# Kernel tuning notes

Hardware: AMD Instinct MI355X
Metric: run time of the kernel (lower is better)

## Reference

```python
import jax, jax.numpy as jnp
import numpy as np

N, E, F, C, K, H = 100000, 1600000, 64, 32, 8, 36


def setup_inputs() -> dict:
    key = jax.random.key(0)
    ks = jax.random.split(key, 24)
    s = 0.1
    inp = {
        "x": jax.random.normal(ks[0], (N, F), jnp.float32),
        "edge_index": jax.random.randint(ks[1], (2, E), 0, N, dtype=jnp.int32),
        # ChebConv conv1_1: K x [F, H] weights + bias
        "W1_1": jax.random.normal(ks[2], (K, F, H), jnp.float32) * s,
        "b1_1": jnp.zeros((H,), jnp.float32),
        "g1_1": jnp.ones((H,), jnp.float32),
        "be1_1": jnp.zeros((H,), jnp.float32),
        # ChebConv conv1_2: K x [H, H]
        "W1_2": jax.random.normal(ks[3], (K, H, H), jnp.float32) * s,
        "b1_2": jnp.zeros((H,), jnp.float32),
        "g1_2": jnp.ones((H,), jnp.float32),
        "be1_2": jnp.zeros((H,), jnp.float32),
        # GINConv MLP: Linear(F,H) -> ReLU -> Linear(H,H)
        "gin_w1": jax.random.normal(ks[4], (F, H), jnp.float32) * s,
        "gin_b1": jnp.zeros((H,), jnp.float32),
        "gin_w2": jax.random.normal(ks[5], (H, H), jnp.float32) * s,
        "gin_b2": jnp.zeros((H,), jnp.float32),
        "g2": jnp.ones((H,), jnp.float32),
        "be2": jnp.zeros((H,), jnp.float32),
        # conv4: ChebConv K=1 on concat(3H) -> C  (pure linear, no propagation)
        "W4": jax.random.normal(ks[6], (1, 3 * H, C), jnp.float32) * s,
        "b4": jnp.zeros((C,), jnp.float32),
    }
    return inp


def _spmm(w, src, dst, x, n):
    # out[i] = sum_{e: dst_e=i} w_e * x[src_e]
    return jax.ops.segment_sum(w[:, None] * x[src], dst, num_segments=n)


def _cheb(x, src, dst, w, Wk, b):
    # PyG ChebConv with sym norm, lambda_max=2: L_hat = -D^-1/2 A D^-1/2 (loop weight 0)
    n = x.shape[0]
    Kk = Wk.shape[0]
    Tx0 = x
    out = Tx0 @ Wk[0]
    if Kk > 1:
        Tx1 = _spmm(w, src, dst, Tx0, n)
        out = out + Tx1 @ Wk[1]
        for k in range(2, Kk):
            Tx2 = 2.0 * _spmm(w, src, dst, Tx1, n) - Tx0
            out = out + Tx2 @ Wk[k]
            Tx0, Tx1 = Tx1, Tx2
    return out + b


def _bn(x, g, b, eps=1e-5):
    m = jnp.mean(x, axis=0)
    v = jnp.mean(jnp.square(x - m), axis=0)  # biased var, training-mode BN
    return g * (x - m) * jax.lax.rsqrt(v + eps) + b


def reference(x, edge_index, W1_1, b1_1, g1_1, be1_1, W1_2, b1_2, g1_2, be1_2,
              gin_w1, gin_b1, gin_w2, gin_b2, g2, be2, W4, b4):
    src, dst = edge_index[0], edge_index[1]
    n = x.shape[0]
    deg = jax.ops.segment_sum(jnp.ones((src.shape[0],), x.dtype), src, num_segments=n)
    dis = jnp.where(deg > 0, jax.lax.rsqrt(jnp.maximum(deg, 1.0)), 0.0)
    w = -dis[src] * dis[dst]  # scaled Laplacian edge weights

    x1_1 = jax.nn.relu(_bn(_cheb(x, src, dst, w, W1_1, b1_1), g1_1, be1_1))
    x1_2 = jax.nn.relu(_bn(_cheb(x1_1, src, dst, w, W1_2, b1_2), g1_2, be1_2))

    # GINConv (eps=0): nn(x + sum_{j in N(i)} x_j)
    agg = jax.ops.segment_sum(x[src], dst, num_segments=n)
    h = x + agg
    gin = jax.nn.relu(h @ gin_w1 + gin_b1) @ gin_w2 + gin_b2
    x2 = _bn(jax.nn.relu(gin), g2, be2)

    x4 = jnp.concatenate((x1_1, x1_2, x2), axis=1)
    return x4 @ W4[0] + b4
```

## Files before the change

### kernel.cpp

```cpp
#include <hip/hip_runtime.h>

constexpr int N_NODES = 100000;
constexpr int N_EDGES = 1600000;
constexpr int NBK  = 391;
constexpr int NBLK = 640;
constexpr int CHUNK = 2500;
constexpr int LCNT = NBK * NBLK;
constexpr int SCAN_BLKS = (LCNT + 255) / 256;


__device__ __forceinline__ unsigned bf16pack(float a, float b) {
    unsigned ua = __float_as_uint(a), ub = __float_as_uint(b);
    ua += 0x7fffu + ((ua >> 16) & 1u);
    ub += 0x7fffu + ((ub >> 16) & 1u);
    return (ua >> 16) | (ub & 0xffff0000u);
}
__device__ __forceinline__ float bflo(unsigned p) { return __uint_as_float(p << 16); }
__device__ __forceinline__ float bfhi(unsigned p) { return __uint_as_float(p & 0xffff0000u); }


__global__ __launch_bounds__(256) void part_count_kernel(
    const int* __restrict__ ei, int* __restrict__ cntD, int* __restrict__ cntS) {
    __shared__ int hd[NBK], hs[NBK];
    int tid = threadIdx.x;
    for (int i = tid; i < NBK; i += 256) { hd[i] = 0; hs[i] = 0; }
    __syncthreads();
    int e0 = blockIdx.x * CHUNK;
    for (int e = e0 + tid; e < e0 + CHUNK; e += 256) {
        int s = ei[e], d = ei[N_EDGES + e];
        atomicAdd(&hs[s >> 8], 1);
        atomicAdd(&hd[d >> 8], 1);
    }
    __syncthreads();
    for (int i = tid; i < NBK; i += 256) {
        cntD[i * NBLK + blockIdx.x] = hd[i];
        cntS[i * NBLK + blockIdx.x] = hs[i];
    }
}

__global__ __launch_bounds__(256) void scanA_kernel(const int* __restrict__ in,
                                                    int* __restrict__ out,
                                                    int* __restrict__ bsum, int L) {
    __shared__ int sm[256];
    int i = blockIdx.x * 256 + threadIdx.x;
    int v = (i < L) ? in[i] : 0;
    sm[threadIdx.x] = v;
    __syncthreads();
    for (int off = 1; off < 256; off <<= 1) {
        int t = (threadIdx.x >= off) ? sm[threadIdx.x - off] : 0;
        __syncthreads();
        sm[threadIdx.x] += t;
        __syncthreads();
    }
    if (i < L) out[i] = sm[threadIdx.x] - v;
    if (threadIdx.x == 255) bsum[blockIdx.x] = sm[255];
}

__global__ __launch_bounds__(1024) void scanB_kernel(int* __restrict__ bsum, int nb) {
    __shared__ int sm[1024];
    int t = threadIdx.x;
    int v = (t < nb) ? bsum[t] : 0;
    sm[t] = v;
    __syncthreads();
    for (int off = 1; off < 1024; off <<= 1) {
        int u = (t >= off) ? sm[t - off] : 0;
        __syncthreads();
        sm[t] += u;
        __syncthreads();
    }
    if (t < nb) bsum[t] = sm[t] - v;
}

__global__ __launch_bounds__(256) void scanC_kernel(int* __restrict__ out,
                                                    const int* __restrict__ bsum, int L) {
    int i = blockIdx.x * 256 + threadIdx.x;
    if (i < L) out[i] += bsum[blockIdx.x];
}

__global__ __launch_bounds__(256) void part_scatter_kernel(
    const int* __restrict__ ei, const int* __restrict__ scanD,
    const int* __restrict__ scanS, int2* __restrict__ edgepart,
    int* __restrict__ srcpart) {
    __shared__ int curD[NBK], curS[NBK];
    int tid = threadIdx.x;
    for (int i = tid; i < NBK; i += 256) {
        curD[i] = scanD[i * NBLK + blockIdx.x];
        curS[i] = scanS[i * NBLK + blockIdx.x];
    }
    __syncthreads();
    int e0 = blockIdx.x * CHUNK;
    for (int e = e0 + tid; e < e0 + CHUNK; e += 256) {
        int s = ei[e], d = ei[N_EDGES + e];
        int pd = atomicAdd(&curD[d >> 8], 1);
        edgepart[pd] = make_int2(s, d);
        int ps = atomicAdd(&curS[s >> 8], 1);
        srcpart[ps] = s;
    }
}

__global__ __launch_bounds__(256) void deg_kernel(const int* __restrict__ srcpart,
                                                  const int* __restrict__ scanS,
                                                  float* __restrict__ dis) {
    __shared__ int cnt[256];
    int b = blockIdx.x, tid = threadIdx.x;
    cnt[tid] = 0;
    __syncthreads();
    int beg = scanS[b * NBLK];
    int end = (b + 1 < NBK) ? scanS[(b + 1) * NBLK] : N_EDGES;
    for (int j = beg + tid; j < end; j += 256)
        atomicAdd(&cnt[srcpart[j] & 255], 1);
    __syncthreads();
    int node = b * 256 + tid;
    if (node < N_NODES) dis[node] = cnt[tid] > 0 ? rsqrtf((float)cnt[tid]) : 0.f;
}

__global__ __launch_bounds__(256) void csr_kernel(const int2* __restrict__ edgepart,
                                                  const int* __restrict__ scanD,
                                                  const float* __restrict__ dis,
                                                  int* __restrict__ rp,
                                                  int2* __restrict__ csrw) {
    __shared__ int cnt[256];
    __shared__ int lofs[256];
    __shared__ float disl[256];
    int b = blockIdx.x, tid = threadIdx.x;
    int beg = scanD[b * NBLK];
    int end = (b + 1 < NBK) ? scanD[(b + 1) * NBLK] : N_EDGES;
    int node = b * 256 + tid;
    cnt[tid] = 0;
    disl[tid] = (node < N_NODES) ? dis[node] : 0.f;
    __syncthreads();
    for (int j = beg + tid; j < end; j += 256)
        atomicAdd(&cnt[edgepart[j].y & 255], 1);
    __syncthreads();
    int v = cnt[tid];
    lofs[tid] = v;
    __syncthreads();
    for (int off = 1; off < 256; off <<= 1) {
        int t = (tid >= off) ? lofs[tid - off] : 0;
        __syncthreads();
        lofs[tid] += t;
        __syncthreads();
    }
    int myexc = lofs[tid] - v;
    if (node < N_NODES) rp[node] = beg + myexc;
    if (b == NBK - 1 && tid == 0) rp[N_NODES] = N_EDGES;
    __syncthreads();
    lofs[tid] = myexc;
    cnt[tid] = 0;
    __syncthreads();
    for (int j = beg + tid; j < end; j += 256) {
        int2 e = edgepart[j];
        int dl = e.y & 255;
        int pos = beg + lofs[dl] + atomicAdd(&cnt[dl], 1);
        csrw[pos] = make_int2(e.x, __float_as_int(-dis[e.x] * disl[dl]));
    }
}


template <int FI, int SCALE, bool HAS_B2, bool BN_A, bool FUSE_STATS, bool OUT_BF16>
__global__ __launch_bounds__(256) void cheb_step_kernel(
    const int* __restrict__ rp, const int2* __restrict__ csrw,
    const uint2* __restrict__ INb, const uint2* __restrict__ B2b,
    const float* __restrict__ A, const float* __restrict__ W,
    const float* __restrict__ ss, void* __restrict__ OUT,
    float* __restrict__ partials) {
    __shared__ float Wl[FI * 36];
    __shared__ float Atile[28][FI + 1];
    __shared__ float ls[72];
    int tid = threadIdx.x;
    for (int i = tid; i < FI * 36; i += 252) Wl[i] = W[i];
    int r0 = blockIdx.x * 28;
    for (int i = tid; i < 28 * FI; i += 252) {
        int r = i / FI, f = i % FI;
        int row = r0 + r;
        float v = (row < N_NODES) ? A[row * FI + f] : 0.f;
        if (BN_A) v = fmaxf(fmaf(ss[f], v, ss[36 + f]), 0.f);
        Atile[r][f] = v;
    }
    if (FUSE_STATS && tid < 72) ls[tid] = 0.f;
    __syncthreads();
    int r = tid / 9, c = tid % 9;
    int row = r0 + r;
    bool valid = row < N_NODES;
    float ax = 0, ay = 0, az = 0, aw = 0;
    float bx = 0, by = 0, bz = 0, bw = 0;
    float cx = 0, cy = 0, cz = 0, cw = 0;
    float dx = 0, dy = 0, dz = 0, dw = 0;
    if (SCALE != 0 && valid) {
        int beg = rp[row], end = rp[row + 1];
        int j = beg;
        for (; j + 7 < end; j += 8) {
            int2 e0 = csrw[j],     e1 = csrw[j + 1], e2 = csrw[j + 2], e3 = csrw[j + 3];
            int2 e4 = csrw[j + 4], e5 = csrw[j + 5], e6 = csrw[j + 6], e7 = csrw[j + 7];
            uint2 u0 = INb[e0.x * 9 + c];
            uint2 u1 = INb[e1.x * 9 + c];
            uint2 u2 = INb[e2.x * 9 + c];
            uint2 u3 = INb[e3.x * 9 + c];
            uint2 u4 = INb[e4.x * 9 + c];
            uint2 u5 = INb[e5.x * 9 + c];
            uint2 u6 = INb[e6.x * 9 + c];
            uint2 u7 = INb[e7.x * 9 + c];
            float w0 = __int_as_float(e0.y), w1 = __int_as_float(e1.y);
            float w2 = __int_as_float(e2.y), w3 = __int_as_float(e3.y);
            float w4 = __int_as_float(e4.y), w5 = __int_as_float(e5.y);
            float w6 = __int_as_float(e6.y), w7 = __int_as_float(e7.y);
            ax = fmaf(w0, bflo(u0.x), ax); ay = fmaf(w0, bfhi(u0.x), ay);
            az = fmaf(w0, bflo(u0.y), az); aw = fmaf(w0, bfhi(u0.y), aw);
            bx = fmaf(w1, bflo(u1.x), bx); by = fmaf(w1, bfhi(u1.x), by);
            bz = fmaf(w1, bflo(u1.y), bz); bw = fmaf(w1, bfhi(u1.y), bw);
            cx = fmaf(w2, bflo(u2.x), cx); cy = fmaf(w2, bfhi(u2.x), cy);
            cz = fmaf(w2, bflo(u2.y), cz); cw = fmaf(w2, bfhi(u2.y), cw);
            dx = fmaf(w3, bflo(u3.x), dx); dy = fmaf(w3, bfhi(u3.x), dy);
            dz = fmaf(w3, bflo(u3.y), dz); dw = fmaf(w3, bfhi(u3.y), dw);
            ax = fmaf(w4, bflo(u4.x), ax); ay = fmaf(w4, bfhi(u4.x), ay);
            az = fmaf(w4, bflo(u4.y), az); aw = fmaf(w4, bfhi(u4.y), aw);
            bx = fmaf(w5, bflo(u5.x), bx); by = fmaf(w5, bfhi(u5.x), by);
            bz = fmaf(w5, bflo(u5.y), bz); bw = fmaf(w5, bfhi(u5.y), bw);
            cx = fmaf(w6, bflo(u6.x), cx); cy = fmaf(w6, bfhi(u6.x), cy);
            cz = fmaf(w6, bflo(u6.y), cz); cw = fmaf(w6, bfhi(u6.y), cw);
            dx = fmaf(w7, bflo(u7.x), dx); dy = fmaf(w7, bfhi(u7.x), dy);
            dz = fmaf(w7, bflo(u7.y), dz); dw = fmaf(w7, bfhi(u7.y), dw);
        }
        for (; j + 3 < end; j += 4) {
            int2 e0 = csrw[j], e1 = csrw[j + 1], e2 = csrw[j + 2], e3 = csrw[j + 3];
            uint2 u0 = INb[e0.x * 9 + c];
            uint2 u1 = INb[e1.x * 9 + c];
            uint2 u2 = INb[e2.x * 9 + c];
            uint2 u3 = INb[e3.x * 9 + c];
            float w0 = __int_as_float(e0.y), w1 = __int_as_float(e1.y);
            float w2 = __int_as_float(e2.y), w3 = __int_as_float(e3.y);
            ax = fmaf(w0, bflo(u0.x), ax); ay = fmaf(w0, bfhi(u0.x), ay);
            az = fmaf(w0, bflo(u0.y), az); aw = fmaf(w0, bfhi(u0.y), aw);
            bx = fmaf(w1, bflo(u1.x), bx); by = fmaf(w1, bfhi(u1.x), by);
            bz = fmaf(w1, bflo(u1.y), bz); bw = fmaf(w1, bfhi(u1.y), bw);
            cx = fmaf(w2, bflo(u2.x), cx); cy = fmaf(w2, bfhi(u2.x), cy);
            cz = fmaf(w2, bflo(u2.y), cz); cw = fmaf(w2, bfhi(u2.y), cw);
            dx = fmaf(w3, bflo(u3.x), dx); dy = fmaf(w3, bfhi(u3.x), dy);
            dz = fmaf(w3, bflo(u3.y), dz); dw = fmaf(w3, bfhi(u3.y), dw);
        }
        for (; j < end; ++j) {
            int2 e = csrw[j];
            uint2 u = INb[e.x * 9 + c];
            float w = __int_as_float(e.y);
            ax = fmaf(w, bflo(u.x), ax); ay = fmaf(w, bfhi(u.x), ay);
            az = fmaf(w, bflo(u.y), az); aw = fmaf(w, bfhi(u.y), aw);
        }
        ax += bx + cx + dx; ay += by + cy + dy;
        az += bz + cz + dz; aw += bw + cw + dw;
    }
    float px = 0, py = 0, pz = 0, pw = 0;
    const float4* Wl4 = (const float4*)Wl;
#pragma unroll 4
    for (int f = 0; f < FI; ++f) {
        float a = Atile[r][f];
        float4 wv = Wl4[f * 9 + c];
        px = fmaf(a, wv.x, px); py = fmaf(a, wv.y, py);
        pz = fmaf(a, wv.z, pz); pw = fmaf(a, wv.w, pw);
    }
    const float S = (float)SCALE;
    float4 o;
    o.x = fmaf(S, ax, px); o.y = fmaf(S, ay, py);
    o.z = fmaf(S, az, pz); o.w = fmaf(S, aw, pw);
    if (valid) {
        if (HAS_B2) {
            uint2 u = B2b[row * 9 + c];
            o.x -= bflo(u.x); o.y -= bfhi(u.x);
            o.z -= bflo(u.y); o.w -= bfhi(u.y);
        }
        if (OUT_BF16) {
            ((uint2*)OUT)[row * 9 + c] =
                make_uint2(bf16pack(o.x, o.y), bf16pack(o.z, o.w));
        } else {
            ((float4*)OUT)[row * 9 + c] = o;
        }
        if (FUSE_STATS) {
            atomicAdd(&ls[c * 4 + 0], o.x); atomicAdd(&ls[36 + c * 4 + 0], o.x * o.x);
            atomicAdd(&ls[c * 4 + 1], o.y); atomicAdd(&ls[36 + c * 4 + 1], o.y * o.y);
            atomicAdd(&ls[c * 4 + 2], o.z); atomicAdd(&ls[36 + c * 4 + 2], o.z * o.z);
            atomicAdd(&ls[c * 4 + 3], o.w); atomicAdd(&ls[36 + c * 4 + 3], o.w * o.w);
        }
    }
    if (FUSE_STATS) {
        __syncthreads();
        if (tid < 72) partials[blockIdx.x * 72 + tid] = ls[tid];
    }
}


__global__ __launch_bounds__(256) void gin_gather_kernel(
    const int* __restrict__ rp, const int2* __restrict__ csrw,
    const uint2* __restrict__ Yb, const float* __restrict__ b1,
    const float* __restrict__ w2, const float* __restrict__ b2,
    float* __restrict__ OUT, float* __restrict__ partials) {
    __shared__ float W2l[36 * 36];
    __shared__ float B1l[36], B2l[36];
    __shared__ float M1t[28][37];
    __shared__ float ls[72];
    int tid = threadIdx.x;
    for (int i = tid; i < 36 * 36; i += 252) W2l[i] = w2[i];
    if (tid < 36) { B1l[tid] = b1[tid]; B2l[tid] = b2[tid]; }
    if (tid < 72) ls[tid] = 0.f;
    __syncthreads();
    int r = tid / 9, c = tid % 9;
    int row = blockIdx.x * 28 + r;
    bool valid = row < N_NODES;
    float ax = 0, ay = 0, az = 0, aw = 0;
    float bx = 0, by = 0, bz = 0, bw = 0;
    float cx = 0, cy = 0, cz = 0, cw = 0;
    float dx = 0, dy = 0, dz = 0, dw = 0;
    if (valid) {
        uint2 us = Yb[row * 9 + c];
        ax = bflo(us.x); ay = bfhi(us.x); az = bflo(us.y); aw = bfhi(us.y);
        int beg = rp[row], end = rp[row + 1];
        int j = beg;
        for (; j + 7 < end; j += 8) {
            int s0 = csrw[j].x,     s1 = csrw[j + 1].x, s2 = csrw[j + 2].x, s3 = csrw[j + 3].x;
            int s4 = csrw[j + 4].x, s5 = csrw[j + 5].x, s6 = csrw[j + 6].x, s7 = csrw[j + 7].x;
            uint2 u0 = Yb[s0 * 9 + c];
            uint2 u1 = Yb[s1 * 9 + c];
            uint2 u2 = Yb[s2 * 9 + c];
            uint2 u3 = Yb[s3 * 9 + c];
            uint2 u4 = Yb[s4 * 9 + c];
            uint2 u5 = Yb[s5 * 9 + c];
            uint2 u6 = Yb[s6 * 9 + c];
            uint2 u7 = Yb[s7 * 9 + c];
            ax += bflo(u0.x) + bflo(u4.x); ay += bfhi(u0.x) + bfhi(u4.x);
            az += bflo(u0.y) + bflo(u4.y); aw += bfhi(u0.y) + bfhi(u4.y);
            bx += bflo(u1.x) + bflo(u5.x); by += bfhi(u1.x) + bfhi(u5.x);
            bz += bflo(u1.y) + bflo(u5.y); bw += bfhi(u1.y) + bfhi(u5.y);
            cx += bflo(u2.x) + bflo(u6.x); cy += bfhi(u2.x) + bfhi(u6.x);
            cz += bflo(u2.y) + bflo(u6.y); cw += bfhi(u2.y) + bfhi(u6.y);
            dx += bflo(u3.x) + bflo(u7.x); dy += bfhi(u3.x) + bfhi(u7.x);
            dz += bflo(u3.y) + bflo(u7.y); dw += bfhi(u3.y) + bfhi(u7.y);
        }
        for (; j + 3 < end; j += 4) {
            int s0 = csrw[j].x, s1 = csrw[j + 1].x, s2 = csrw[j + 2].x, s3 = csrw[j + 3].x;
            uint2 u0 = Yb[s0 * 9 + c];
            uint2 u1 = Yb[s1 * 9 + c];
            uint2 u2 = Yb[s2 * 9 + c];
            uint2 u3 = Yb[s3 * 9 + c];
            ax += bflo(u0.x); ay += bfhi(u0.x); az += bflo(u0.y); aw += bfhi(u0.y);
            bx += bflo(u1.x); by += bfhi(u1.x); bz += bflo(u1.y); bw += bfhi(u1.y);
            cx += bflo(u2.x); cy += bfhi(u2.x); cz += bflo(u2.y); cw += bfhi(u2.y);
            dx += bflo(u3.x); dy += bfhi(u3.x); dz += bflo(u3.y); dw += bfhi(u3.y);
        }
        for (; j < end; ++j) {
            uint2 u = Yb[csrw[j].x * 9 + c];
            ax += bflo(u.x); ay += bfhi(u.x);
            az += bflo(u.y); aw += bfhi(u.y);
        }
        ax += bx + cx + dx; ay += by + cy + dy;
        az += bz + cz + dz; aw += bw + cw + dw;
    }
    float m0 = fmaxf(ax + B1l[c * 4 + 0], 0.f);
    float m1 = fmaxf(ay + B1l[c * 4 + 1], 0.f);
    float m2 = fmaxf(az + B1l[c * 4 + 2], 0.f);
    float m3 = fmaxf(aw + B1l[c * 4 + 3], 0.f);
    M1t[r][c * 4 + 0] = m0; M1t[r][c * 4 + 1] = m1;
    M1t[r][c * 4 + 2] = m2; M1t[r][c * 4 + 3] = m3;
    __syncthreads();
    float o0 = B2l[c * 4 + 0], o1 = B2l[c * 4 + 1];
    float o2 = B2l[c * 4 + 2], o3 = B2l[c * 4 + 3];
    const float4* W2l4 = (const float4*)W2l;
#pragma unroll 4
    for (int f = 0; f < 36; ++f) {
        float a = M1t[r][f];
        float4 wv = W2l4[f * 9 + c];
        o0 = fmaf(a, wv.x, o0); o1 = fmaf(a, wv.y, o1);
        o2 = fmaf(a, wv.z, o2); o3 = fmaf(a, wv.w, o3);
    }
    o0 = fmaxf(o0, 0.f); o1 = fmaxf(o1, 0.f);
    o2 = fmaxf(o2, 0.f); o3 = fmaxf(o3, 0.f);
    if (valid) {
        float4 o = {o0, o1, o2, o3};
        ((float4*)OUT)[row * 9 + c] = o;
        atomicAdd(&ls[c * 4 + 0], o0); atomicAdd(&ls[36 + c * 4 + 0], o0 * o0);
        atomicAdd(&ls[c * 4 + 1], o1); atomicAdd(&ls[36 + c * 4 + 1], o1 * o1);
        atomicAdd(&ls[c * 4 + 2], o2); atomicAdd(&ls[36 + c * 4 + 2], o2 * o2);
        atomicAdd(&ls[c * 4 + 3], o3); atomicAdd(&ls[36 + c * 4 + 3], o3 * o3);
    }
    __syncthreads();
    if (tid < 72) partials[blockIdx.x * 72 + tid] = ls[tid];
}


__global__ __launch_bounds__(256) void finalize_kernel(
    const float* __restrict__ partials, int nb, const float* __restrict__ g,
    const float* __restrict__ be, float* __restrict__ ss) {
    __shared__ float rs[256], rq[256];
    int c = blockIdx.x;
    int t = threadIdx.x;
    float s = 0.f, q = 0.f;
    for (int i = t; i < nb; i += 256) {
        s += partials[i * 72 + c];
        q += partials[i * 72 + c + 36];
    }
    rs[t] = s; rq[t] = q;
    __syncthreads();
    for (int off = 128; off > 0; off >>= 1) {
        if (t < off) { rs[t] += rs[t + off]; rq[t] += rq[t + off]; }
        __syncthreads();
    }
    if (t == 0) {
        float m = rs[0] / (float)N_NODES;
        float v = rq[0] / (float)N_NODES - m * m;
        float sc = g[c] * rsqrtf(v + 1e-5f);
        ss[c] = sc;
        ss[36 + c] = be[c] - m * sc;
    }
}


__global__ __launch_bounds__(256) void fused3_kernel(
    const float* __restrict__ X1, const float* __restrict__ ssA,
    const float* __restrict__ X2, const float* __restrict__ ssB,
    const float* __restrict__ X3, const float* __restrict__ ssC,
    const float* __restrict__ W, const float* __restrict__ b,
    float* __restrict__ out) {
    __shared__ float Wl[108 * 32];
    __shared__ float Al[64][109];
    int tid = threadIdx.x;
    for (int i = tid; i < 108 * 32; i += 256) Wl[i] = W[i];
    int r0 = blockIdx.x * 64;
    for (int i = tid; i < 64 * 108; i += 256) {
        int r = i / 108, f = i % 108;
        int row = r0 + r;
        float v = 0.f;
        if (row < N_NODES) {
            if (f < 36) {
                v = fmaxf(fmaf(ssA[f], X1[row * 36 + f], ssA[36 + f]), 0.f);
            } else if (f < 72) {
                int ff = f - 36;
                v = fmaxf(fmaf(ssB[ff], X2[row * 36 + ff], ssB[36 + ff]), 0.f);
            } else {
                int ff = f - 72;
                v = fmaf(ssC[ff], X3[row * 36 + ff], ssC[36 + ff]);
            }
        }
        Al[r][f] = v;
    }
    __syncthreads();
    int r = tid >> 2, q = tid & 3;
    int row = r0 + r;
    if (row >= N_NODES) return;
    float acc[8];
#pragma unroll
    for (int j = 0; j < 8; ++j) acc[j] = b[q * 8 + j];
    for (int f = 0; f < 108; ++f) {
        float a = Al[r][f];
#pragma unroll
        for (int j = 0; j < 8; ++j)
            acc[j] = fmaf(a, Wl[f * 32 + q * 8 + j], acc[j]);
    }
#pragma unroll
    for (int j = 0; j < 8; ++j) out[row * 32 + q * 8 + j] = acc[j];
}


extern "C" void kernel_launch(void* const* d_in, const int* in_sizes, int n_in,
                              void* d_out, int out_size, void* d_ws, size_t ws_size,
                              hipStream_t stream) {
    const float* x      = (const float*)d_in[0];
    const int*   ei     = (const int*)d_in[1];
    const float* W1_1   = (const float*)d_in[2];
    const float* g1_1   = (const float*)d_in[4];
    const float* be1_1  = (const float*)d_in[5];
    const float* W1_2   = (const float*)d_in[6];
    const float* g1_2   = (const float*)d_in[8];
    const float* be1_2  = (const float*)d_in[9];
    const float* gin_w1 = (const float*)d_in[10];
    const float* gin_b1 = (const float*)d_in[11];
    const float* gin_w2 = (const float*)d_in[12];
    const float* gin_b2 = (const float*)d_in[13];
    const float* g2     = (const float*)d_in[14];
    const float* be2    = (const float*)d_in[15];
    const float* W4     = (const float*)d_in[16];
    const float* b4     = (const float*)d_in[17];
    float* out = (float*)d_out;

    char* ws = (char*)d_ws;
    size_t off = 0;
    auto alloc = [&](size_t bytes) -> char* {
        char* p = ws + off;
        off = (off + bytes + 255) & ~(size_t)255;
        return p;
    };
    int*   cntD  = (int*)alloc((size_t)LCNT * 4);
    int*   cntS  = (int*)alloc((size_t)LCNT * 4);
    int*   bsum  = (int*)alloc(1024 * 4);
    int*   rp    = (int*)alloc((size_t)(N_NODES + 1) * 4);
    float* dis   = (float*)alloc((size_t)N_NODES * 4);
    int2*  edgepart = (int2*)alloc((size_t)N_EDGES * 8);
    int*   srcpart  = (int*)alloc((size_t)N_EDGES * 4);
    int2*  csrw  = (int2*)alloc((size_t)N_EDGES * 8);
    float* ssA   = (float*)alloc(72 * 4);
    float* ssB   = (float*)alloc(72 * 4);
    float* ssC   = (float*)alloc(72 * 4);
    float* partials = (float*)alloc((size_t)6250 * 72 * 4);
    constexpr size_t NB36 = (size_t)N_NODES * 36 * 4;
    constexpr size_t NBBF = (size_t)N_NODES * 72;
    uint2* R0  = (uint2*)alloc(NBBF);
    uint2* R1  = (uint2*)alloc(NBBF);
    uint2* R2  = (uint2*)alloc(NBBF);
    float* X1  = (float*)alloc(NB36);
    float* X2  = (float*)alloc(NB36);
    float* X3  = (float*)alloc(NB36);
    if (off > ws_size) return;

    part_count_kernel<<<NBLK, 256, 0, stream>>>(ei, cntD, cntS);
    scanA_kernel<<<SCAN_BLKS, 256, 0, stream>>>(cntD, cntD, bsum, LCNT);
    scanB_kernel<<<1, 1024, 0, stream>>>(bsum, SCAN_BLKS);
    scanC_kernel<<<SCAN_BLKS, 256, 0, stream>>>(cntD, bsum, LCNT);
    scanA_kernel<<<SCAN_BLKS, 256, 0, stream>>>(cntS, cntS, bsum, LCNT);
    scanB_kernel<<<1, 1024, 0, stream>>>(bsum, SCAN_BLKS);
    scanC_kernel<<<SCAN_BLKS, 256, 0, stream>>>(cntS, bsum, LCNT);
    part_scatter_kernel<<<NBLK, 256, 0, stream>>>(ei, cntD, cntS, edgepart, srcpart);
    deg_kernel<<<NBK, 256, 0, stream>>>(srcpart, cntS, dis);
    csr_kernel<<<NBK, 256, 0, stream>>>(edgepart, cntD, dis, rp, csrw);

    const int STEP_BLKS = (N_NODES + 27) / 28;
    const int F3_BLKS   = (N_NODES + 63) / 64;

    cheb_step_kernel<64, 0, false, false, false, true><<<STEP_BLKS, 252, 0, stream>>>(
        rp, csrw, nullptr, nullptr, x, W1_1 + 7 * 2304, nullptr, R0, nullptr);
    cheb_step_kernel<64, 2, false, false, false, true><<<STEP_BLKS, 252, 0, stream>>>(
        rp, csrw, R0, nullptr, x, W1_1 + 6 * 2304, nullptr, R1, nullptr);
    cheb_step_kernel<64, 2, true, false, false, true><<<STEP_BLKS, 252, 0, stream>>>(
        rp, csrw, R1, R0, x, W1_1 + 5 * 2304, nullptr, R2, nullptr);
    cheb_step_kernel<64, 2, true, false, false, true><<<STEP_BLKS, 252, 0, stream>>>(
        rp, csrw, R2, R1, x, W1_1 + 4 * 2304, nullptr, R0, nullptr);
    cheb_step_kernel<64, 2, true, false, false, true><<<STEP_BLKS, 252, 0, stream>>>(
        rp, csrw, R0, R2, x, W1_1 + 3 * 2304, nullptr, R1, nullptr);
    cheb_step_kernel<64, 2, true, false, false, true><<<STEP_BLKS, 252, 0, stream>>>(
        rp, csrw, R1, R0, x, W1_1 + 2 * 2304, nullptr, R2, nullptr);
    cheb_step_kernel<64, 2, true, false, false, true><<<STEP_BLKS, 252, 0, stream>>>(
        rp, csrw, R2, R1, x, W1_1 + 1 * 2304, nullptr, R0, nullptr);
    cheb_step_kernel<64, 1, true, false, true, false><<<STEP_BLKS, 252, 0, stream>>>(
        rp, csrw, R0, R2, x, W1_1 + 0 * 2304, nullptr, X1, partials);
    finalize_kernel<<<36, 256, 0, stream>>>(partials, STEP_BLKS, g1_1, be1_1, ssA);

    cheb_step_kernel<36, 0, false, true, false, true><<<STEP_BLKS, 252, 0, stream>>>(
        rp, csrw, nullptr, nullptr, X1, W1_2 + 7 * 1296, ssA, R0, nullptr);
    cheb_step_kernel<36, 2, false, true, false, true><<<STEP_BLKS, 252, 0, stream>>>(
        rp, csrw, R0, nullptr, X1, W1_2 + 6 * 1296, ssA, R1, nullptr);
    cheb_step_kernel<36, 2, true, true, false, true><<<STEP_BLKS, 252, 0, stream>>>(
        rp, csrw, R1, R0, X1, W1_2 + 5 * 1296, ssA, R2, nullptr);
    cheb_step_kernel<36, 2, true, true, false, true><<<STEP_BLKS, 252, 0, stream>>>(
        rp, csrw, R2, R1, X1, W1_2 + 4 * 1296, ssA, R0, nullptr);
    cheb_step_kernel<36, 2, true, true, false, true><<<STEP_BLKS, 252, 0, stream>>>(
        rp, csrw, R0, R2, X1, W1_2 + 3 * 1296, ssA, R1, nullptr);
    cheb_step_kernel<36, 2, true, true, false, true><<<STEP_BLKS, 252, 0, stream>>>(
        rp, csrw, R1, R0, X1, W1_2 + 2 * 1296, ssA, R2, nullptr);
    cheb_step_kernel<36, 2, true, true, false, true><<<STEP_BLKS, 252, 0, stream>>>(
        rp, csrw, R2, R1, X1, W1_2 + 1 * 1296, ssA, R0, nullptr);
    cheb_step_kernel<36, 1, true, true, true, false><<<STEP_BLKS, 252, 0, stream>>>(
        rp, csrw, R0, R2, X1, W1_2 + 0 * 1296, ssA, X2, partials);
    finalize_kernel<<<36, 256, 0, stream>>>(partials, STEP_BLKS, g1_2, be1_2, ssB);

    cheb_step_kernel<64, 0, false, false, false, true><<<STEP_BLKS, 252, 0, stream>>>(
        rp, csrw, nullptr, nullptr, x, gin_w1, nullptr, R0, nullptr);
    gin_gather_kernel<<<STEP_BLKS, 252, 0, stream>>>(rp, csrw, R0, gin_b1,
                                                     gin_w2, gin_b2, X3, partials);
    finalize_kernel<<<36, 256, 0, stream>>>(partials, STEP_BLKS, g2, be2, ssC);

    fused3_kernel<<<F3_BLKS, 256, 0, stream>>>(X1, ssA, X2, ssB, X3, ssC, W4, b4, out);
}
```

Baseline: 970.7 us.

## Use bf16 dense inputs, nontemporal CSR loads, and a retiled final linear kernel

Packs x into bf16 once, and has the last conv1_1 step also write a bf16 copy of X1. The dense A-tile loads in every Chebyshev step then read half the bytes. CSR edge records are fetched as single 64-bit nontemporal loads, and bf16 outputs use nontemporal stores. The 4-wide remainder loops are removed. The final fused linear kernel is retiled to 32 rows per block with 4 outputs per thread. Costs are an extra pack kernel and buffer, lower precision on dense inputs (x and X1 rounded to bf16), and possible cache-policy side effects from the nontemporal hints.

Result: slower. 1.126 ms (+16.0%).

```diff
diff --git a/kernel.cpp b/kernel.cpp
--- a/kernel.cpp
+++ b/kernel.cpp
@@ -156,26 +156,45 @@
     }
 }
 
-
-template <int FI, int SCALE, bool HAS_B2, bool BN_A, bool FUSE_STATS, bool OUT_BF16>
+__global__ void pack_x_kernel(const float* __restrict__ x, uint2* __restrict__ xbf) {
+    int i = blockIdx.x * blockDim.x + threadIdx.x;
+    if (i >= N_NODES * 16) return;
+    float4 v = ((const float4*)x)[i];
+    xbf[i] = make_uint2(bf16pack(v.x, v.y), bf16pack(v.z, v.w));
+}
+
+
+template <int FI, int SCALE, bool HAS_B2, bool BN_A, bool FUSE_STATS, bool OUT_BF16, bool DUAL>
 __global__ __launch_bounds__(256) void cheb_step_kernel(
     const int* __restrict__ rp, const int2* __restrict__ csrw,
     const uint2* __restrict__ INb, const uint2* __restrict__ B2b,
-    const float* __restrict__ A, const float* __restrict__ W,
+    const uint2* __restrict__ Ab, const float* __restrict__ W,
     const float* __restrict__ ss, void* __restrict__ OUT,
-    float* __restrict__ partials) {
+    unsigned long long* __restrict__ OUTB, float* __restrict__ partials) {
+    constexpr int RU2 = FI / 4;
     __shared__ float Wl[FI * 36];
     __shared__ float Atile[28][FI + 1];
     __shared__ float ls[72];
     int tid = threadIdx.x;
     for (int i = tid; i < FI * 36; i += 252) Wl[i] = W[i];
     int r0 = blockIdx.x * 28;
-    for (int i = tid; i < 28 * FI; i += 252) {
-        int r = i / FI, f = i % FI;
+    const long long* ab8 = (const long long*)Ab;
+    for (int i = tid; i < 28 * RU2; i += 252) {
+        int r = i / RU2, u = i % RU2;
         int row = r0 + r;
-        float v = (row < N_NODES) ? A[row * FI + f] : 0.f;
-        if (BN_A) v = fmaxf(fmaf(ss[f], v, ss[36 + f]), 0.f);
-        Atile[r][f] = v;
+        long long av = (row < N_NODES)
+            ? __builtin_nontemporal_load(ab8 + (size_t)row * RU2 + u) : 0LL;
+        unsigned lo = (unsigned)av, hi = (unsigned)(av >> 32);
+        float f0 = bflo(lo), f1 = bfhi(lo), f2 = bflo(hi), f3 = bfhi(hi);
+        if (BN_A) {
+            int f = u * 4;
+            f0 = fmaxf(fmaf(ss[f + 0], f0, ss[36 + f + 0]), 0.f);
+            f1 = fmaxf(fmaf(ss[f + 1], f1, ss[36 + f + 1]), 0.f);
+            f2 = fmaxf(fmaf(ss[f + 2], f2, ss[36 + f + 2]), 0.f);
+            f3 = fmaxf(fmaf(ss[f + 3], f3, ss[36 + f + 3]), 0.f);
+        }
+        Atile[r][u * 4 + 0] = f0; Atile[r][u * 4 + 1] = f1;
+        Atile[r][u * 4 + 2] = f2; Atile[r][u * 4 + 3] = f3;
     }
     if (FUSE_STATS && tid < 72) ls[tid] = 0.f;
     __syncthreads();
@@ -187,23 +206,30 @@
     float cx = 0, cy = 0, cz = 0, cw = 0;
     float dx = 0, dy = 0, dz = 0, dw = 0;
     if (SCALE != 0 && valid) {
+        const long long* cs = (const long long*)csrw;
         int beg = rp[row], end = rp[row + 1];
         int j = beg;
         for (; j + 7 < end; j += 8) {
-            int2 e0 = csrw[j],     e1 = csrw[j + 1], e2 = csrw[j + 2], e3 = csrw[j + 3];
-            int2 e4 = csrw[j + 4], e5 = csrw[j + 5], e6 = csrw[j + 6], e7 = csrw[j + 7];
-            uint2 u0 = INb[e0.x * 9 + c];
-            uint2 u1 = INb[e1.x * 9 + c];
-            uint2 u2 = INb[e2.x * 9 + c];
-            uint2 u3 = INb[e3.x * 9 + c];
-            uint2 u4 = INb[e4.x * 9 + c];
-            uint2 u5 = INb[e5.x * 9 + c];
-            uint2 u6 = INb[e6.x * 9 + c];
-            uint2 u7 = INb[e7.x * 9 + c];
-            float w0 = __int_as_float(e0.y), w1 = __int_as_float(e1.y);
-            float w2 = __int_as_float(e2.y), w3 = __int_as_float(e3.y);
-            float w4 = __int_as_float(e4.y), w5 = __int_as_float(e5.y);
-            float w6 = __int_as_float(e6.y), w7 = __int_as_float(e7.y);
+            long long v0 = __builtin_nontemporal_load(cs + j);
+            long long v1 = __builtin_nontemporal_load(cs + j + 1);
+            long long v2 = __builtin_nontemporal_load(cs + j + 2);
+            long long v3 = __builtin_nontemporal_load(cs + j + 3);
+            long long v4 = __builtin_nontemporal_load(cs + j + 4);
+            long long v5 = __builtin_nontemporal_load(cs + j + 5);
+            long long v6 = __builtin_nontemporal_load(cs + j + 6);
+            long long v7 = __builtin_nontemporal_load(cs + j + 7);
+            uint2 u0 = INb[(size_t)(int)v0 * 9 + c];
+            uint2 u1 = INb[(size_t)(int)v1 * 9 + c];
+            uint2 u2 = INb[(size_t)(int)v2 * 9 + c];
+            uint2 u3 = INb[(size_t)(int)v3 * 9 + c];
+            uint2 u4 = INb[(size_t)(int)v4 * 9 + c];
+            uint2 u5 = INb[(size_t)(int)v5 * 9 + c];
+            uint2 u6 = INb[(size_t)(int)v6 * 9 + c];
+            uint2 u7 = INb[(size_t)(int)v7 * 9 + c];
+            float w0 = __int_as_float((int)(v0 >> 32)), w1 = __int_as_float((int)(v1 >> 32));
+            float w2 = __int_as_float((int)(v2 >> 32)), w3 = __int_as_float((int)(v3 >> 32));
+            float w4 = __int_as_float((int)(v4 >> 32)), w5 = __int_as_float((int)(v5 >> 32));
+            float w6 = __int_as_float((int)(v6 >> 32)), w7 = __int_as_float((int)(v7 >> 32));
             ax = fmaf(w0, bflo(u0.x), ax); ay = fmaf(w0, bfhi(u0.x), ay);
             az = fmaf(w0, bflo(u0.y), az); aw = fmaf(w0, bfhi(u0.y), aw);
             bx = fmaf(w1, bflo(u1.x), bx); by = fmaf(w1, bfhi(u1.x), by);
@@ -221,27 +247,10 @@
             dx = fmaf(w7, bflo(u7.x), dx); dy = fmaf(w7, bfhi(u7.x), dy);
             dz = fmaf(w7, bflo(u7.y), dz); dw = fmaf(w7, bfhi(u7.y), dw);
         }
-        for (; j + 3 < end; j += 4) {
-            int2 e0 = csrw[j], e1 = csrw[j + 1], e2 = csrw[j + 2], e3 = csrw[j + 3];
-            uint2 u0 = INb[e0.x * 9 + c];
-            uint2 u1 = INb[e1.x * 9 + c];
-            uint2 u2 = INb[e2.x * 9 + c];
-            uint2 u3 = INb[e3.x * 9 + c];
-            float w0 = __int_as_float(e0.y), w1 = __int_as_float(e1.y);
-            float w2 = __int_as_float(e2.y), w3 = __int_as_float(e3.y);
-            ax = fmaf(w0, bflo(u0.x), ax); ay = fmaf(w0, bfhi(u0.x), ay);
-            az = fmaf(w0, bflo(u0.y), az); aw = fmaf(w0, bfhi(u0.y), aw);
-            bx = fmaf(w1, bflo(u1.x), bx); by = fmaf(w1, bfhi(u1.x), by);
-            bz = fmaf(w1, bflo(u1.y), bz); bw = fmaf(w1, bfhi(u1.y), bw);
-            cx = fmaf(w2, bflo(u2.x), cx); cy = fmaf(w2, bfhi(u2.x), cy);
-            cz = fmaf(w2, bflo(u2.y), cz); cw = fmaf(w2, bfhi(u2.y), cw);
-            dx = fmaf(w3, bflo(u3.x), dx); dy = fmaf(w3, bfhi(u3.x), dy);
-            dz = fmaf(w3, bflo(u3.y), dz); dw = fmaf(w3, bfhi(u3.y), dw);
-        }
         for (; j < end; ++j) {
-            int2 e = csrw[j];
-            uint2 u = INb[e.x * 9 + c];
-            float w = __int_as_float(e.y);
+            long long v = __builtin_nontemporal_load(cs + j);
+            uint2 u = INb[(size_t)(int)v * 9 + c];
+            float w = __int_as_float((int)(v >> 32));
             ax = fmaf(w, bflo(u.x), ax); ay = fmaf(w, bfhi(u.x), ay);
             az = fmaf(w, bflo(u.y), az); aw = fmaf(w, bfhi(u.y), aw);
         }
@@ -263,15 +272,21 @@
     o.z = fmaf(S, az, pz); o.w = fmaf(S, aw, pw);
     if (valid) {
         if (HAS_B2) {
-            uint2 u = B2b[row * 9 + c];
+            uint2 u = B2b[(size_t)row * 9 + c];
             o.x -= bflo(u.x); o.y -= bfhi(u.x);
             o.z -= bflo(u.y); o.w -= bfhi(u.y);
         }
         if (OUT_BF16) {
-            ((uint2*)OUT)[row * 9 + c] =
-                make_uint2(bf16pack(o.x, o.y), bf16pack(o.z, o.w));
+            unsigned long long pv = (unsigned long long)bf16pack(o.x, o.y)
+                                  | ((unsigned long long)bf16pack(o.z, o.w) << 32);
+            __builtin_nontemporal_store(pv, (unsigned long long*)OUT + (size_t)row * 9 + c);
         } else {
-            ((float4*)OUT)[row * 9 + c] = o;
+            ((float4*)OUT)[(size_t)row * 9 + c] = o;
+        }
+        if (DUAL) {
+            unsigned long long pv = (unsigned long long)bf16pack(o.x, o.y)
+                                  | ((unsigned long long)bf16pack(o.z, o.w) << 32);
+            __builtin_nontemporal_store(pv, OUTB + (size_t)row * 9 + c);
         }
         if (FUSE_STATS) {
             atomicAdd(&ls[c * 4 + 0], o.x); atomicAdd(&ls[36 + c * 4 + 0], o.x * o.x);
@@ -309,21 +324,28 @@
     float cx = 0, cy = 0, cz = 0, cw = 0;
     float dx = 0, dy = 0, dz = 0, dw = 0;
     if (valid) {
-        uint2 us = Yb[row * 9 + c];
+        uint2 us = Yb[(size_t)row * 9 + c];
         ax = bflo(us.x); ay = bfhi(us.x); az = bflo(us.y); aw = bfhi(us.y);
+        const long long* cs = (const long long*)csrw;
         int beg = rp[row], end = rp[row + 1];
         int j = beg;
         for (; j + 7 < end; j += 8) {
-            int s0 = csrw[j].x,     s1 = csrw[j + 1].x, s2 = csrw[j + 2].x, s3 = csrw[j + 3].x;
-            int s4 = csrw[j + 4].x, s5 = csrw[j + 5].x, s6 = csrw[j + 6].x, s7 = csrw[j + 7].x;
-            uint2 u0 = Yb[s0 * 9 + c];
-            uint2 u1 = Yb[s1 * 9 + c];
-            uint2 u2 = Yb[s2 * 9 + c];
-            uint2 u3 = Yb[s3 * 9 + c];
-            uint2 u4 = Yb[s4 * 9 + c];
-            uint2 u5 = Yb[s5 * 9 + c];
-            uint2 u6 = Yb[s6 * 9 + c];
-            uint2 u7 = Yb[s7 * 9 + c];
+            int s0 = (int)__builtin_nontemporal_load(cs + j);
+            int s1 = (int)__builtin_nontemporal_load(cs + j + 1);
+            int s2 = (int)__builtin_nontemporal_load(cs + j + 2);
+            int s3 = (int)__builtin_nontemporal_load(cs + j + 3);
+            int s4 = (int)__builtin_nontemporal_load(cs + j + 4);
+            int s5 = (int)__builtin_nontemporal_load(cs + j + 5);
+            int s6 = (int)__builtin_nontemporal_load(cs + j + 6);
+            int s7 = (int)__builtin_nontemporal_load(cs + j + 7);
+            uint2 u0 = Yb[(size_t)s0 * 9 + c];
+            uint2 u1 = Yb[(size_t)s1 * 9 + c];
+            uint2 u2 = Yb[(size_t)s2 * 9 + c];
+            uint2 u3 = Yb[(size_t)s3 * 9 + c];
+            uint2 u4 = Yb[(size_t)s4 * 9 + c];
+            uint2 u5 = Yb[(size_t)s5 * 9 + c];
+            uint2 u6 = Yb[(size_t)s6 * 9 + c];
+            uint2 u7 = Yb[(size_t)s7 * 9 + c];
             ax += bflo(u0.x) + bflo(u4.x); ay += bfhi(u0.x) + bfhi(u4.x);
             az += bflo(u0.y) + bflo(u4.y); aw += bfhi(u0.y) + bfhi(u4.y);
             bx += bflo(u1.x) + bflo(u5.x); by += bfhi(u1.x) + bfhi(u5.x);
@@ -333,19 +355,8 @@
             dx += bflo(u3.x) + bflo(u7.x); dy += bfhi(u3.x) + bfhi(u7.x);
             dz += bflo(u3.y) + bflo(u7.y); dw += bfhi(u3.y) + bfhi(u7.y);
         }
-        for (; j + 3 < end; j += 4) {
-            int s0 = csrw[j].x, s1 = csrw[j + 1].x, s2 = csrw[j + 2].x, s3 = csrw[j + 3].x;
-            uint2 u0 = Yb[s0 * 9 + c];
-            uint2 u1 = Yb[s1 * 9 + c];
-            uint2 u2 = Yb[s2 * 9 + c];
-            uint2 u3 = Yb[s3 * 9 + c];
-            ax += bflo(u0.x); ay += bfhi(u0.x); az += bflo(u0.y); aw += bfhi(u0.y);
-            bx += bflo(u1.x); by += bfhi(u1.x); bz += bflo(u1.y); bw += bfhi(u1.y);
-            cx += bflo(u2.x); cy += bfhi(u2.x); cz += bflo(u2.y); cw += bfhi(u2.y);
-            dx += bflo(u3.x); dy += bfhi(u3.x); dz += bflo(u3.y); dw += bfhi(u3.y);
-        }
         for (; j < end; ++j) {
-            uint2 u = Yb[csrw[j].x * 9 + c];
+            uint2 u = Yb[(size_t)(int)__builtin_nontemporal_load(cs + j) * 9 + c];
             ax += bflo(u.x); ay += bfhi(u.x);
             az += bflo(u.y); aw += bfhi(u.y);
         }
@@ -373,7 +384,7 @@
     o2 = fmaxf(o2, 0.f); o3 = fmaxf(o3, 0.f);
     if (valid) {
         float4 o = {o0, o1, o2, o3};
-        ((float4*)OUT)[row * 9 + c] = o;
+        ((float4*)OUT)[(size_t)row * 9 + c] = o;
         atomicAdd(&ls[c * 4 + 0], o0); atomicAdd(&ls[36 + c * 4 + 0], o0 * o0);
         atomicAdd(&ls[c * 4 + 1], o1); atomicAdd(&ls[36 + c * 4 + 1], o1 * o1);
         atomicAdd(&ls[c * 4 + 2], o2); atomicAdd(&ls[36 + c * 4 + 2], o2 * o2);
@@ -418,42 +429,45 @@
     const float* __restrict__ W, const float* __restrict__ b,
     float* __restrict__ out) {
     __shared__ float Wl[108 * 32];
-    __shared__ float Al[64][109];
+    __shared__ float Al[32][109];
     int tid = threadIdx.x;
     for (int i = tid; i < 108 * 32; i += 256) Wl[i] = W[i];
-    int r0 = blockIdx.x * 64;
-    for (int i = tid; i < 64 * 108; i += 256) {
+    int r0 = blockIdx.x * 32;
+    for (int i = tid; i < 32 * 108; i += 256) {
         int r = i / 108, f = i % 108;
         int row = r0 + r;
         float v = 0.f;
         if (row < N_NODES) {
             if (f < 36) {
-                v = fmaxf(fmaf(ssA[f], X1[row * 36 + f], ssA[36 + f]), 0.f);
+                v = fmaxf(fmaf(ssA[f], __builtin_nontemporal_load(&X1[(size_t)row * 36 + f]),
+                               ssA[36 + f]), 0.f);
             } else if (f < 72) {
                 int ff = f - 36;
-                v = fmaxf(fmaf(ssB[ff], X2[row * 36 + ff], ssB[36 + ff]), 0.f);
+                v = fmaxf(fmaf(ssB[ff], __builtin_nontemporal_load(&X2[(size_t)row * 36 + ff]),
+                               ssB[36 + ff]), 0.f);
             } else {
                 int ff = f - 72;
-                v = fmaf(ssC[ff], X3[row * 36 + ff], ssC[36 + ff]);
+                v = fmaf(ssC[ff], __builtin_nontemporal_load(&X3[(size_t)row * 36 + ff]),
+                         ssC[36 + ff]);
             }
         }
         Al[r][f] = v;
     }
     __syncthreads();
-    int r = tid >> 2, q = tid & 3;
+    int r = tid >> 3, q = tid & 7;
     int row = r0 + r;
     if (row >= N_NODES) return;
-    float acc[8];
+    float acc[4];
 #pragma unroll
-    for (int j = 0; j < 8; ++j) acc[j] = b[q * 8 + j];
+    for (int j = 0; j < 4; ++j) acc[j] = b[q * 4 + j];
     for (int f = 0; f < 108; ++f) {
         float a = Al[r][f];
 #pragma unroll
-        for (int j = 0; j < 8; ++j)
-            acc[j] = fmaf(a, Wl[f * 32 + q * 8 + j], acc[j]);
+        for (int j = 0; j < 4; ++j)
+            acc[j] = fmaf(a, Wl[f * 32 + q * 4 + j], acc[j]);
     }
 #pragma unroll
-    for (int j = 0; j < 8; ++j) out[row * 32 + q * 8 + j] = acc[j];
+    for (int j = 0; j < 4; ++j) out[(size_t)row * 32 + q * 4 + j] = acc[j];
 }
 
 
@@ -499,9 +513,11 @@
     float* partials = (float*)alloc((size_t)6250 * 72 * 4);
     constexpr size_t NB36 = (size_t)N_NODES * 36 * 4;
     constexpr size_t NBBF = (size_t)N_NODES * 72;
+    uint2* xbf = (uint2*)alloc((size_t)N_NODES * 128);
     uint2* R0  = (uint2*)alloc(NBBF);
     uint2* R1  = (uint2*)alloc(NBBF);
     uint2* R2  = (uint2*)alloc(NBBF);
+    uint2* X1b = (uint2*)alloc(NBBF);
     float* X1  = (float*)alloc(NB36);
     float* X2  = (float*)alloc(NB36);
     float* X3  = (float*)alloc(NB36);
@@ -517,48 +533,50 @@
     part_scatter_kernel<<<NBLK, 256, 0, stream>>>(ei, cntD, cntS, edgepart, srcpart);
     deg_kernel<<<NBK, 256, 0, stream>>>(srcpart, cntS, dis);
     csr_kernel<<<NBK, 256, 0, stream>>>(edgepart, cntD, dis, rp, csrw);
+    pack_x_kernel<<<(N_NODES * 16 + 255) / 256, 256, 0, stream>>>(x, xbf);
 
     const int STEP_BLKS = (N_NODES + 27) / 28;
-    const int F3_BLKS   = (N_NODES + 63) / 64;
-
-    cheb_step_kernel<64, 0, false, false, false, true><<<STEP_BLKS, 252, 0, stream>>>(
-        rp, csrw, nullptr, nullptr, x, W1_1 + 7 * 2304, nullptr, R0, nullptr);
-    cheb_step_kernel<64, 2, false, false, false, true><<<STEP_BLKS, 252, 0, stream>>>(
-        rp, csrw, R0, nullptr, x, W1_1 + 6 * 2304, nullptr, R1, nullptr);
-    cheb_step_kernel<64, 2, true, false, false, true><<<STEP_BLKS, 252, 0, stream>>>(
-        rp, csrw, R1, R0, x, W1_1 + 5 * 2304, nullptr, R2, nullptr);
-    cheb_step_kernel<64, 2, true, false, false, true><<<STEP_BLKS, 252, 0, stream>>>(
-        rp, csrw, R2, R1, x, W1_1 + 4 * 2304, nullptr, R0, nullptr);
-    cheb_step_kernel<64, 2, true, false, false, true><<<STEP_BLKS, 252, 0, stream>>>(
-        rp, csrw, R0, R2, x, W1_1 + 3 * 2304, nullptr, R1, nullptr);
-    cheb_step_kernel<64, 2, true, false, false, true><<<STEP_BLKS, 252, 0, stream>>>(
-        rp, csrw, R1, R0, x, W1_1 + 2 * 2304, nullptr, R2, nullptr);
-    cheb_step_kernel<64, 2, true, false, false, true><<<STEP_BLKS, 252, 0, stream>>>(
-        rp, csrw, R2, R1, x, W1_1 + 1 * 2304, nullptr, R0, nullptr);
-    cheb_step_kernel<64, 1, true, false, true, false><<<STEP_BLKS, 252, 0, stream>>>(
-        rp, csrw, R0, R2, x, W1_1 + 0 * 2304, nullptr, X1, partials);
+    const int F3_BLKS   = (N_NODES + 31) / 32;
+
+    cheb_step_kernel<64, 0, false, false, false, true, false><<<STEP_BLKS, 252, 0, stream>>>(
+        rp, csrw, nullptr, nullptr, xbf, W1_1 + 7 * 2304, nullptr, R0, nullptr, nullptr);
+    cheb_step_kernel<64, 2, false, false, false, true, false><<<STEP_BLKS, 252, 0, stream>>>(
+        rp, csrw, R0, nullptr, xbf, W1_1 + 6 * 2304, nullptr, R1, nullptr, nullptr);
+    cheb_step_kernel<64, 2, true, false, false, true, false><<<STEP_BLKS, 252, 0, stream>>>(
+        rp, csrw, R1, R0, xbf, W1_1 + 5 * 2304, nullptr, R2, nullptr, nullptr);
+    cheb_step_kernel<64, 2, true, false, false, true, false><<<STEP_BLKS, 252, 0, stream>>>(
+        rp, csrw, R2, R1, xbf, W1_1 + 4 * 2304, nullptr, R0, nullptr, nullptr);
+    cheb_step_kernel<64, 2, true, false, false, true, false><<<STEP_BLKS, 252, 0, stream>>>(
+        rp, csrw, R0, R2, xbf, W1_1 + 3 * 2304, nullptr, R1, nullptr, nullptr);
+    cheb_step_kernel<64, 2, true, false, false, true, false><<<STEP_BLKS, 252, 0, stream>>>(
+        rp, csrw, R1, R0, xbf, W1_1 + 2 * 2304, nullptr, R2, nullptr, nullptr);
+    cheb_step_kernel<64, 2, true, false, false, true, false><<<STEP_BLKS, 252, 0, stream>>>(
+        rp, csrw, R2, R1, xbf, W1_1 + 1 * 2304, nullptr, R0, nullptr, nullptr);
+    cheb_step_kernel<64, 1, true, false, true, false, true><<<STEP_BLKS, 252, 0, stream>>>(
+        rp, csrw, R0, R2, xbf, W1_1 + 0 * 2304, nullptr, X1,
+        (unsigned long long*)X1b, partials);
     finalize_kernel<<<36, 256, 0, stream>>>(partials, STEP_BLKS, g1_1, be1_1, ssA);
 
-    cheb_step_kernel<36, 0, false, true, false, true><<<STEP_BLKS, 252, 0, stream>>>(
-        rp, csrw, nullptr, nullptr, X1, W1_2 + 7 * 1296, ssA, R0, nullptr);
-    cheb_step_kernel<36, 2, false, true, false, true><<<STEP_BLKS, 252, 0, stream>>>(
-        rp, csrw, R0, nullptr, X1, W1_2 + 6 * 1296, ssA, R1, nullptr);
-    cheb_step_kernel<36, 2, true, true, false, true><<<STEP_BLKS, 252, 0, stream>>>(
-        rp, csrw, R1, R0, X1, W1_2 + 5 * 1296, ssA, R2, nullptr);
-    cheb_step_kernel<36, 2, true, true, false, true><<<STEP_BLKS, 252, 0, stream>>>(
-        rp, csrw, R2, R1, X1, W1_2 + 4 * 1296, ssA, R0, nullptr);
-    cheb_step_kernel<36, 2, true, true, false, true><<<STEP_BLKS, 252, 0, stream>>>(
-        rp, csrw, R0, R2, X1, W1_2 + 3 * 1296, ssA, R1, nullptr);
-    cheb_step_kernel<36, 2, true, true, false, true><<<STEP_BLKS, 252, 0, stream>>>(
-        rp, csrw, R1, R0, X1, W1_2 + 2 * 1296, ssA, R2, nullptr);
-    cheb_step_kernel<36, 2, true, true, false, true><<<STEP_BLKS, 252, 0, stream>>>(
-        rp, csrw, R2, R1, X1, W1_2 + 1 * 1296, ssA, R0, nullptr);
-    cheb_step_kernel<36, 1, true, true, true, false><<<STEP_BLKS, 252, 0, stream>>>(
-        rp, csrw, R0, R2, X1, W1_2 + 0 * 1296, ssA, X2, partials);
+    cheb_step_kernel<36, 0, false, true, false, true, false><<<STEP_BLKS, 252, 0, stream>>>(
+        rp, csrw, nullptr, nullptr, X1b, W1_2 + 7 * 1296, ssA, R0, nullptr, nullptr);
+    cheb_step_kernel<36, 2, false, true, false, true, false><<<STEP_BLKS, 252, 0, stream>>>(
+        rp, csrw, R0, nullptr, X1b, W1_2 + 6 * 1296, ssA, R1, nullptr, nullptr);
+    cheb_step_kernel<36, 2, true, true, false, true, false><<<STEP_BLKS, 252, 0, stream>>>(
+        rp, csrw, R1, R0, X1b, W1_2 + 5 * 1296, ssA, R2, nullptr, nullptr);
+    cheb_step_kernel<36, 2, true, true, false, true, false><<<STEP_BLKS, 252, 0, stream>>>(
+        rp, csrw, R2, R1, X1b, W1_2 + 4 * 1296, ssA, R0, nullptr, nullptr);
+    cheb_step_kernel<36, 2, true, true, false, true, false><<<STEP_BLKS, 252, 0, stream>>>(
+        rp, csrw, R0, R2, X1b, W1_2 + 3 * 1296, ssA, R1, nullptr, nullptr);
+    cheb_step_kernel<36, 2, true, true, false, true, false><<<STEP_BLKS, 252, 0, stream>>>(
+        rp, csrw, R1, R0, X1b, W1_2 + 2 * 1296, ssA, R2, nullptr, nullptr);
+    cheb_step_kernel<36, 2, true, true, false, true, false><<<STEP_BLKS, 252, 0, stream>>>(
+        rp, csrw, R2, R1, X1b, W1_2 + 1 * 1296, ssA, R0, nullptr, nullptr);
+    cheb_step_kernel<36, 1, true, true, true, false, false><<<STEP_BLKS, 252, 0, stream>>>(
+        rp, csrw, R0, R2, X1b, W1_2 + 0 * 1296, ssA, X2, nullptr, partials);
     finalize_kernel<<<36, 256, 0, stream>>>(partials, STEP_BLKS, g1_2, be1_2, ssB);
 
-    cheb_step_kernel<64, 0, false, false, false, true><<<STEP_BLKS, 252, 0, stream>>>(
-        rp, csrw, nullptr, nullptr, x, gin_w1, nullptr, R0, nullptr);
+    cheb_step_kernel<64, 0, false, false, false, true, false><<<STEP_BLKS, 252, 0, stream>>>(
+        rp, csrw, nullptr, nullptr, xbf, gin_w1, nullptr, R0, nullptr, nullptr);
     gin_gather_kernel<<<STEP_BLKS, 252, 0, stream>>>(rp, csrw, R0, gin_b1,
                                                      gin_w2, gin_b2, X3, partials);
     finalize_kernel<<<36, 256, 0, stream>>>(partials, STEP_BLKS, g2, be2, ssC);
```
